# Kernel optimization log

Hardware: AMD Instinct MI355X
Metric: run time of the kernel (lower is better)

## Reference

```python
import jax, jax.numpy as jnp
import numpy as np

DIM = 1024
NH = 16        # query heads
NKV = 4        # kv heads
HD = 64        # head dim
GROUPS = NH // NKV
SPATIAL = 16
NZ = SPATIAL * SPATIAL  # 256 latent tokens with 2D structure
SOFT_CAP = 50.0
SCALE = HD ** -0.5
EPS = 1e-6


def rope_2d_cos_sin(nz, hd, spatial, dtype):
    # 2D RoPE: first half of head_dim encodes row position, second half column.
    pos = jnp.arange(nz)
    row = (pos // spatial).astype(jnp.float32)
    col = (pos % spatial).astype(jnp.float32)
    quarter = hd // 4
    inv_freq = 1.0 / (10000.0 ** (jnp.arange(quarter, dtype=jnp.float32) / quarter))
    f_row = row[:, None] * inv_freq[None, :]   # (nz, hd/4)
    f_col = col[:, None] * inv_freq[None, :]   # (nz, hd/4)
    emb = jnp.concatenate([f_row, f_col], axis=-1)      # (nz, hd/2)
    emb = jnp.concatenate([emb, emb], axis=-1)          # (nz, hd)
    return jnp.cos(emb).astype(dtype), jnp.sin(emb).astype(dtype)


def rotate_half(x):
    x1, x2 = jnp.split(x, 2, axis=-1)
    return jnp.concatenate([-x2, x1], axis=-1)


def apply_rotary(x, cos, sin):
    return x * cos + rotate_half(x) * sin


def rms_norm(x, w):
    # RMSNorm over head_dim with learned per-dim scale (QKNorm)
    return x * jax.lax.rsqrt(jnp.mean(x * x, axis=-1, keepdims=True) + EPS) * w


def setup_inputs() -> dict:
    key = jax.random.key(0)
    ks = jax.random.split(key, 7)
    B, T, S = 4, 16, 264
    x = jax.random.normal(ks[0], (B, T, S, DIM), dtype=jnp.float32)
    wq = jax.random.normal(ks[1], (NH * HD, DIM), dtype=jnp.float32) * 0.02
    wk = jax.random.normal(ks[2], (NKV * HD, DIM), dtype=jnp.float32) * 0.02
    wv = jax.random.normal(ks[3], (NKV * HD, DIM), dtype=jnp.float32) * 0.02
    wo = jax.random.normal(ks[4], (DIM, NH * HD), dtype=jnp.float32) * 0.02
    q_norm_w = jnp.ones((HD,), dtype=jnp.float32)
    k_norm_w = jnp.ones((HD,), dtype=jnp.float32)
    return {"x": x, "wq": wq, "wk": wk, "wv": wv, "wo": wo,
            "q_norm_w": q_norm_w, "k_norm_w": k_norm_w}


def reference(x, wq, wk, wv, wo, q_norm_w, k_norm_w):
    B, T, S, D = x.shape
    xf = x.reshape(B * T, S, D)
    # projections (torch Linear: y = x @ W.T)
    q = (xf @ wq.T).reshape(B * T, S, NH, HD).transpose(0, 2, 1, 3)   # (BT,NH,S,HD)
    k = (xf @ wk.T).reshape(B * T, S, NKV, HD).transpose(0, 2, 1, 3)  # (BT,NKV,S,HD)
    v = (xf @ wv.T).reshape(B * T, S, NKV, HD).transpose(0, 2, 1, 3)
    # QKNorm
    q = rms_norm(q, q_norm_w)
    k = rms_norm(k, k_norm_w)
    # partial 2D RoPE on latent tokens only
    cos, sin = rope_2d_cos_sin(NZ, HD, SPATIAL, q.dtype)
    cos = cos[None, None]  # (1,1,NZ,HD)
    sin = sin[None, None]
    q = jnp.concatenate([apply_rotary(q[:, :, :NZ], cos, sin), q[:, :, NZ:]], axis=2)
    k = jnp.concatenate([apply_rotary(k[:, :, :NZ], cos, sin), k[:, :, NZ:]], axis=2)
    # GQA: expand kv heads (repeat_interleave == jnp.repeat)
    k = jnp.repeat(k, GROUPS, axis=1)
    v = jnp.repeat(v, GROUPS, axis=1)
    # attention with soft cap
    attn = jnp.einsum("bhqd,bhkd->bhqk", q, k) * SCALE
    attn = SOFT_CAP * jnp.tanh(attn / SOFT_CAP)
    attn = jax.nn.softmax(attn, axis=-1)
    out = jnp.einsum("bhqk,bhkd->bhqd", attn, v)
    out = out.transpose(0, 2, 1, 3).reshape(B * T, S, NH * HD)
    out = out @ wo.T
    return out.reshape(B, T, S, D)
```

## Files before the change

### kernel.cpp

```cpp
#include <hip/hip_runtime.h>

typedef __bf16 bf16;
typedef __bf16 bf16x8 __attribute__((ext_vector_type(8)));
typedef float  f32x4  __attribute__((ext_vector_type(4)));
typedef float  f32x16 __attribute__((ext_vector_type(16)));
typedef unsigned int u32;

#define DIM   1024
#define NH    16
#define NKV   4
#define HD    64
#define SLEN  264
#define BTOT  64
#define MROWS (BTOT * SLEN)
#define NQKV  1536
#define NZ    256
#define VPAD  288

__device__ __forceinline__ void gl_lds16(const bf16* g, bf16* l) {
    __builtin_amdgcn_global_load_lds((__attribute__((address_space(1))) void*)(g),
                                     (__attribute__((address_space(3))) void*)(l),
                                     16, 0, 0);
}

__global__ void cvt_f32_bf16(const float* __restrict__ src, bf16* __restrict__ dst, int n) {
    int i = (blockIdx.x * 256 + threadIdx.x) * 4;
    if (i < n) {
        float4 v = *(const float4*)(src + i);
        dst[i + 0] = (bf16)v.x; dst[i + 1] = (bf16)v.y;
        dst[i + 2] = (bf16)v.z; dst[i + 3] = (bf16)v.w;
    }
}

__global__ void prep_misc(const float* __restrict__ wq, const float* __restrict__ wk,
                          const float* __restrict__ wv, const float* __restrict__ wo,
                          bf16* __restrict__ wcat, bf16* __restrict__ wobf,
                          float2* __restrict__ ctab) {
    int b = blockIdx.x, tid = threadIdx.x;
    if (b < 1536) {
        int i = (b * 256 + tid) * 4;
        const float* src; int off;
        if (i < 1024 * 1024)      { src = wq; off = i; }
        else if (i < 1280 * 1024) { src = wk; off = i - 1024 * 1024; }
        else                      { src = wv; off = i - 1280 * 1024; }
        float4 v = *(const float4*)(src + off);
        wcat[i + 0] = (bf16)v.x; wcat[i + 1] = (bf16)v.y;
        wcat[i + 2] = (bf16)v.z; wcat[i + 3] = (bf16)v.w;
    } else if (b < 2560) {
        int i = ((b - 1536) * 256 + tid) * 4;
        float4 v = *(const float4*)(wo + i);
        wobf[i + 0] = (bf16)v.x; wobf[i + 1] = (bf16)v.y;
        wobf[i + 2] = (bf16)v.z; wobf[i + 3] = (bf16)v.w;
    } else {
        int i = (b - 2560) * 256 + tid;
        int s = i >> 5, d = i & 31;
        const float LN1 = 0.5756462732485115f;
        float pos = (d < 16) ? (float)(s >> 4) : (float)(s & 15);
        float ang = pos * expf(-(float)(d & 15) * LN1);
        float sn, cs; sincosf(ang, &sn, &cs);
        ctab[i] = make_float2(cs, sn);
    }
}

__device__ __forceinline__ int xcd_swizzle(int orig, int nwg) {
    int q = nwg >> 3, r = nwg & 7;
    int xcd = orig & 7, lid = orig >> 3;
    return (xcd < r ? xcd * (q + 1) : r * (q + 1) + (xcd - r) * q) + lid;
}


#define GATE2  asm volatile("s_waitcnt vmcnt(2)" ::: "memory")
#define NOGATE do {} while (0)

#define STAGE(DST, G, H, KT) do {                                              \
    gl_lds16((G) + (size_t)((H) * 128 + rs0) * DIM + (KT) * 64 + cs0 * 8,      \
             (DST) + wid * 512);                                               \
    gl_lds16((G) + (size_t)((H) * 128 + 64 + rs0) * DIM + (KT) * 64 + cs0 * 8, \
             (DST) + 4096 + wid * 512);                                        \
} while (0)

#define PHASE(Ad, Bd, AA, KS, STAGE_STMT, GATE_STMT) do {                      \
    bf16x8 af_[4], bf_[4];                                                     \
    _Pragma("unroll")                                                          \
    for (int i_ = 0; i_ < 4; i_++) {                                           \
        af_[i_] = *(const bf16x8*)((Ad) + aRdBase + i_ * 1024 + xorv[KS]);     \
        bf_[i_] = *(const bf16x8*)((Bd) + bRdBase + i_ * 1024 + xorv[KS]);     \
    }                                                                          \
    STAGE_STMT;                                                                \
    GATE_STMT;                                                                 \
    __builtin_amdgcn_s_barrier();                                              \
    asm volatile("s_waitcnt lgkmcnt(0)" ::: "memory");                         \
    __builtin_amdgcn_sched_barrier(0);                                         \
    __builtin_amdgcn_s_setprio(1);                                             \
    _Pragma("unroll")                                                          \
    for (int i_ = 0; i_ < 4; i_++)                                             \
        _Pragma("unroll")                                                      \
        for (int n_ = 0; n_ < 4; n_++)                                         \
            acc[AA][i_][n_] = __builtin_amdgcn_mfma_f32_16x16x32_bf16(         \
                af_[i_], bf_[n_], acc[AA][i_][n_], 0, 0, 0);                   \
    __builtin_amdgcn_s_setprio(0);                                             \
    __builtin_amdgcn_s_barrier();                                              \
} while (0)

__device__ __forceinline__ void gemm256_core(const bf16* __restrict__ Ag,
                                             const bf16* __restrict__ Bg,
                                             f32x4 (&acc)[2][4][4]) {
    __shared__ __align__(16) bf16 A00[128 * 64], A01[128 * 64], A10[128 * 64], A11[128 * 64];
    __shared__ __align__(16) bf16 B00[128 * 64], B01[128 * 64], B10[128 * 64], B11[128 * 64];

    const int tid  = threadIdx.x;
    const int wid  = tid >> 6, lane = tid & 63;
    const int quad = lane >> 4, r16 = lane & 15;
    const int wm = wid & 1, wn = wid >> 1;

    const int rs0 = tid >> 3;
    const int cs0 = (tid & 7) ^ (rs0 & 7);

    const int aRdBase = (wm * 64 + r16) * 64;
    const int bRdBase = ((wn & 1) * 64 + r16) * 64;
    const int xorv[2] = { (quad ^ (r16 & 7)) * 8, ((4 + quad) ^ (r16 & 7)) * 8 };

    const bf16* Bd0 = (wn & 2) ? B01 : B00;
    const bf16* Bd1 = (wn & 2) ? B11 : B10;

    STAGE(A00, Ag, 0, 0);
    STAGE(A01, Ag, 1, 0);
    STAGE(B00, Bg, 0, 0);
    STAGE(B01, Bg, 1, 0);
    STAGE(A10, Ag, 0, 1);
    GATE2;
    __builtin_amdgcn_s_barrier();

#pragma unroll 1
    for (int it = 0; it < 8; ++it) {
        const int t1 = 2 * it + 1;
        int t2 = 2 * it + 2; if (t2 > 15) t2 = 15;
        int t3 = 2 * it + 3; if (t3 > 15) t3 = 15;
        PHASE(A00, Bd0, 0, 0, STAGE(A11, Ag, 1, t1), NOGATE);
        PHASE(A00, Bd0, 0, 1, STAGE(B10, Bg, 0, t1), NOGATE);
        PHASE(A01, Bd0, 1, 0, STAGE(B11, Bg, 1, t1), NOGATE);
        PHASE(A01, Bd0, 1, 1, STAGE(A00, Ag, 0, t2), GATE2);
        PHASE(A10, Bd1, 0, 0, STAGE(A01, Ag, 1, t2), NOGATE);
        PHASE(A10, Bd1, 0, 1, STAGE(B00, Bg, 0, t2), NOGATE);
        PHASE(A11, Bd1, 1, 0, STAGE(B01, Bg, 1, t2), NOGATE);
        PHASE(A11, Bd1, 1, 1, STAGE(A10, Ag, 0, t3), GATE2);
    }
}

__global__ __launch_bounds__(512) void gemm_qkv(const bf16* __restrict__ A,
                                                const bf16* __restrict__ Bw,
                                                bf16* __restrict__ out,
                                                const float* __restrict__ qw,
                                                const float* __restrict__ kw,
                                                const float2* __restrict__ ctab) {
    const int nwg = (MROWS / 256) * (NQKV / 256);
    int wg = xcd_swizzle(blockIdx.x, nwg);
    const int bm = wg / 6, bn = wg - bm * 6;

    f32x4 acc[2][4][4];
#pragma unroll
    for (int a = 0; a < 2; a++)
#pragma unroll
        for (int i = 0; i < 4; i++)
#pragma unroll
            for (int n = 0; n < 4; n++) acc[a][i][n] = (f32x4){0.f, 0.f, 0.f, 0.f};

    gemm256_core(A + (size_t)bm * 256 * DIM, Bw + (size_t)bn * 256 * DIM, acc);

    const int tid  = threadIdx.x;
    const int wid  = tid >> 6, lane = tid & 63;
    const int quad = lane >> 4, r16 = lane & 15;
    const int wm = wid & 1, wn = wid >> 1;
    const int colbase = bn * 256 + wn * 64;
    const int rowb    = bm * 256 + wm * 64;

    if (bn < 5) {
        const float* w = (bn < 4) ? qw : kw;
        float wreg[4];
#pragma unroll
        for (int n = 0; n < 4; n++) wreg[n] = w[n * 16 + r16];
#pragma unroll
        for (int a = 0; a < 2; a++)
#pragma unroll
            for (int i = 0; i < 4; i++)
#pragma unroll
                for (int r = 0; r < 4; r++) {
                    float ss = 0.f;
#pragma unroll
                    for (int n = 0; n < 4; n++) ss += acc[a][i][n][r] * acc[a][i][n][r];
                    ss += __shfl_xor(ss, 1, 64);
                    ss += __shfl_xor(ss, 2, 64);
                    ss += __shfl_xor(ss, 4, 64);
                    ss += __shfl_xor(ss, 8, 64);
                    float rms = rsqrtf(ss * (1.f / 64.f) + 1e-6f);
                    float xv[4];
#pragma unroll
                    for (int n = 0; n < 4; n++) xv[n] = acc[a][i][n][r] * rms * wreg[n];
                    int gm = rowb + a * 128 + i * 16 + quad * 4 + r;
                    int s = gm % SLEN;
                    if (s < NZ) {
                        float2 cs0 = ctab[s * 32 + r16];
                        float2 cs1 = ctab[s * 32 + 16 + r16];
                        float a0 = xv[0] * cs0.x - xv[2] * cs0.y;
                        float a2 = xv[2] * cs0.x + xv[0] * cs0.y;
                        float a1 = xv[1] * cs1.x - xv[3] * cs1.y;
                        float a3 = xv[3] * cs1.x + xv[1] * cs1.y;
                        xv[0] = a0; xv[1] = a1; xv[2] = a2; xv[3] = a3;
                    }
                    size_t rowoff = (size_t)gm * NQKV + colbase + r16;
#pragma unroll
                    for (int n = 0; n < 4; n++) out[rowoff + n * 16] = (bf16)xv[n];
                }
    } else {
#pragma unroll
        for (int a = 0; a < 2; a++)
#pragma unroll
            for (int i = 0; i < 4; i++)
#pragma unroll
                for (int r = 0; r < 4; r++) {
                    int gm = rowb + a * 128 + i * 16 + quad * 4 + r;
                    size_t rowoff = (size_t)gm * NQKV + colbase + r16;
#pragma unroll
                    for (int n = 0; n < 4; n++) out[rowoff + n * 16] = (bf16)acc[a][i][n][r];
                }
    }
}

#define GEMM_STAGE_PTRS(Mptr, tileRow, K, P)                                   \
    const bf16* P[4];                                                          \
    {                                                                          \
        _Pragma("unroll")                                                      \
        for (int k = 0; k < 4; k++) {                                          \
            int s = k * 256 + tid;                                             \
            int r = s >> 3, cp = s & 7;                                        \
            int c = cp ^ (r & 7);                                              \
            P[k] = (Mptr) + (size_t)((tileRow) + r) * (K) + c * 8;             \
        }                                                                      \
    }

__device__ __forceinline__ int swz(int row, int chunk) {
    return row * 64 + ((chunk ^ (row & 7)) * 8);
}

__global__ __launch_bounds__(256) void gemm_bt(const bf16* __restrict__ A,
                                               const bf16* __restrict__ Bw,
                                               float* __restrict__ Cout) {
    __shared__ __align__(16) bf16 As[128 * 64];
    __shared__ __align__(16) bf16 Bs[128 * 64];
    const int tid  = threadIdx.x;
    const int wid  = tid >> 6, lane = tid & 63;
    const int quad = lane >> 4, r16 = lane & 15;
    const int bid = blockIdx.x;
    const int g = bid / 32, rr = bid - g * 32;
    const int bm = g * 4 + (rr & 3), bn = rr >> 2;
    const int wm = wid & 1, wn = wid >> 1;

    GEMM_STAGE_PTRS(A,  bm * 128, DIM, Ap)
    GEMM_STAGE_PTRS(Bw, bn * 128, DIM, Bp)

    f32x4 acc[4][4];
#pragma unroll
    for (int i = 0; i < 4; i++)
#pragma unroll
        for (int j = 0; j < 4; j++) acc[i][j] = (f32x4){0.f, 0.f, 0.f, 0.f};

    for (int k0 = 0; k0 < DIM; k0 += 64) {
        __syncthreads();
#pragma unroll
        for (int k = 0; k < 4; k++) {
            gl_lds16(Ap[k] + k0, As + (k * 256 + wid * 64) * 8);
            gl_lds16(Bp[k] + k0, Bs + (k * 256 + wid * 64) * 8);
        }
        __syncthreads();
#pragma unroll
        for (int ks = 0; ks < 2; ks++) {
            bf16x8 a[4], b[4];
#pragma unroll
            for (int i = 0; i < 4; i++) {
                a[i] = *(const bf16x8*)&As[swz(wm * 64 + i * 16 + r16, ks * 4 + quad)];
                b[i] = *(const bf16x8*)&Bs[swz(wn * 64 + i * 16 + r16, ks * 4 + quad)];
            }
#pragma unroll
            for (int i = 0; i < 4; i++)
#pragma unroll
                for (int j = 0; j < 4; j++)
                    acc[i][j] = __builtin_amdgcn_mfma_f32_16x16x32_bf16(a[i], b[j], acc[i][j], 0, 0, 0);
        }
    }

#pragma unroll
    for (int i = 0; i < 4; i++)
#pragma unroll
        for (int j = 0; j < 4; j++)
#pragma unroll
            for (int r = 0; r < 4; r++) {
                int gm = bm * 128 + wm * 64 + i * 16 + quad * 4 + r;
                int gn = bn * 128 + wn * 64 + j * 16 + r16;
                Cout[(size_t)gm * DIM + gn] = acc[i][j][r];
            }
}

__global__ __launch_bounds__(256) void vtrans_kernel(const bf16* __restrict__ qkv,
                                                     bf16* __restrict__ vt) {
    __shared__ bf16 Ls[64 * 272];
    const int tid = threadIdx.x;
    const int b = blockIdx.x, bt = b >> 2, kv = b & 3;
    const int part = tid >> 5;
    const int rr   = tid & 31;
#pragma unroll
    for (int pass = 0; pass < 9; ++pass) {
        int row = pass * 32 + rr;
        if (row < SLEN) {
            bf16x8 v = *(const bf16x8*)(qkv + (size_t)(bt * SLEN + row) * NQKV + 1280 + kv * 64 + part * 8);
#pragma unroll
            for (int j = 0; j < 8; j++) Ls[(part * 8 + j) * 272 + row] = v[j];
        }
    }
    __syncthreads();
    const int d = tid >> 2, seg = tid & 3;
    size_t obase = ((size_t)b * 64 + d) * VPAD;
#pragma unroll
    for (int m = 0; m < 9; ++m) {
        int col = seg * 72 + m * 8;
        bf16x8 o;
#pragma unroll
        for (int j = 0; j < 8; j++) {
            int s = col + j;
            o[j] = (s < SLEN) ? Ls[d * 272 + s] : (bf16)0.f;
        }
        *(bf16x8*)(vt + obase + col) = o;
    }
}

__global__ __launch_bounds__(256) void attn_kernel(const bf16* __restrict__ qkv,
                                                   const bf16* __restrict__ vt,
                                                   bf16* __restrict__ aout) {
    __shared__ float invL[4][32];
    const int tid = threadIdx.x;
    const int wid = tid >> 6, lane = tid & 63;
    const int l31 = lane & 31, hi = lane >> 5;
    const int qp = blockIdx.x;
    const int kv = blockIdx.y, bt = blockIdx.z;
    const int h = kv * 4 + wid;

    int q0 = qp * 32 + l31;
    int qcl = q0 < SLEN ? q0 : SLEN - 1;
    const bf16* qbase = qkv + (size_t)(bt * SLEN + qcl) * NQKV + h * HD + hi * 8;
    bf16x8 qb[4];
#pragma unroll
    for (int s = 0; s < 4; s++) qb[s] = *(const bf16x8*)(qbase + s * 16);

    const bf16* kbase = qkv + (size_t)bt * SLEN * NQKV + 1024 + kv * HD + hi * 8;
    const bf16* vbase = vt + (size_t)(bt * 4 + kv) * HD * VPAD;

    bf16x8 nka[4];
    {
        const bf16* kp = kbase + (size_t)l31 * NQKV;
#pragma unroll
        for (int s = 0; s < 4; s++) nka[s] = *(const bf16x8*)(kp + s * 16);
    }

    f32x16 oacc[2];
#pragma unroll
    for (int r = 0; r < 16; r++) { oacc[0][r] = 0.f; oacc[1][r] = 0.f; }
    float lsum = 0.f;

    for (int c = 0; c < 9; ++c) {
        bf16x8 ka[4];
#pragma unroll
        for (int s = 0; s < 4; s++) ka[s] = nka[s];
        if (c < 8) {
            int key = (c + 1) * 32 + l31;
            int kc = key < SLEN ? key : SLEN - 1;
            const bf16* kp = kbase + (size_t)kc * NQKV;
#pragma unroll
            for (int s = 0; s < 4; s++) nka[s] = *(const bf16x8*)(kp + s * 16);
        }
        bf16x8 vb[2][2];
#pragma unroll
        for (int dt = 0; dt < 2; dt++)
#pragma unroll
            for (int st = 0; st < 2; st++)
                vb[dt][st] = *(const bf16x8*)(vbase + (size_t)(dt * 32 + l31) * VPAD + c * 32 + st * 16 + hi * 8);

        f32x16 sacc;
#pragma unroll
        for (int r = 0; r < 16; r++) sacc[r] = 0.f;
#pragma unroll
        for (int s = 0; s < 4; s++)
            sacc = __builtin_amdgcn_mfma_f32_32x32x16_bf16(ka[s], qb[s], sacc, 0, 0, 0);

        float p[16];
#pragma unroll
        for (int r = 0; r < 16; ++r) {
            int key = c * 32 + (r & 3) + 8 * (r >> 2) + 4 * hi;
            float sc = sacc[r];
            float z = sc * 0.0025f;
            float z2 = z * z;
            float poly = fmaf(z2, fmaf(z2, 0.133333333f, -0.333333333f), 1.f);
            float pv = exp2f(sc * 0.18033688f * poly);
            pv = (key < SLEN) ? pv : 0.f;
            p[r] = pv;
            lsum += pv;
        }
#pragma unroll
        for (int st = 0; st < 2; st++) {
            u32 wA, wB, wC, wD;
            asm("v_cvt_pk_bf16_f32 %0, %1, %2" : "=v"(wA) : "v"(p[st*8+0]), "v"(p[st*8+1]));
            asm("v_cvt_pk_bf16_f32 %0, %1, %2" : "=v"(wB) : "v"(p[st*8+2]), "v"(p[st*8+3]));
            asm("v_cvt_pk_bf16_f32 %0, %1, %2" : "=v"(wC) : "v"(p[st*8+4]), "v"(p[st*8+5]));
            asm("v_cvt_pk_bf16_f32 %0, %1, %2" : "=v"(wD) : "v"(p[st*8+6]), "v"(p[st*8+7]));
            asm volatile("v_permlane32_swap_b32 %0, %1" : "+v"(wA), "+v"(wC));
            asm volatile("v_permlane32_swap_b32 %0, %1" : "+v"(wB), "+v"(wD));
            union { u32 u[4]; bf16x8 v; } pa;
            pa.u[0] = wA; pa.u[1] = wB; pa.u[2] = wC; pa.u[3] = wD;
#pragma unroll
            for (int dt = 0; dt < 2; dt++)
                oacc[dt] = __builtin_amdgcn_mfma_f32_32x32x16_bf16(pa.v, vb[dt][st], oacc[dt], 0, 0, 0);
        }
    }

    lsum += __shfl_xor(lsum, 32, 64);
    invL[wid][l31] = 1.f / lsum;
#pragma unroll
    for (int r = 0; r < 16; ++r) {
        int qloc = (r & 3) + 8 * (r >> 2) + 4 * hi;
        int q = qp * 32 + qloc;
        if (q < SLEN) {
            float inv = invL[wid][qloc];
            size_t base = (size_t)(bt * SLEN + q) * (NH * HD) + h * HD + l31;
            aout[base]      = (bf16)(oacc[0][r] * inv);
            aout[base + 32] = (bf16)(oacc[1][r] * inv);
        }
    }
}

extern "C" void kernel_launch(void* const* d_in, const int* in_sizes, int n_in,
                              void* d_out, int out_size, void* d_ws, size_t ws_size,
                              hipStream_t stream) {
    const float* x   = (const float*)d_in[0];
    const float* wq  = (const float*)d_in[1];
    const float* wk  = (const float*)d_in[2];
    const float* wv  = (const float*)d_in[3];
    const float* wo  = (const float*)d_in[4];
    const float* qnw = (const float*)d_in[5];
    const float* knw = (const float*)d_in[6];

    bf16* xbf  = (bf16*)d_ws;
    bf16* wcat = xbf  + (size_t)MROWS * DIM;
    bf16* wobf = wcat + (size_t)NQKV * DIM;
    bf16* qkv  = wobf + (size_t)DIM * DIM;
    bf16* vt   = qkv  + (size_t)MROWS * NQKV;
    float2* ctab = (float2*)(vt + (size_t)BTOT * NKV * HD * VPAD);
    bf16* aout = xbf;

    prep_misc<<<2592, 256, 0, stream>>>(wq, wk, wv, wo, wcat, wobf, ctab);
    cvt_f32_bf16<<<(MROWS * DIM) / 1024, 256, 0, stream>>>(x, xbf, MROWS * DIM);

    gemm_qkv<<<(MROWS / 256) * (NQKV / 256), 512, 0, stream>>>(xbf, wcat, qkv, qnw, knw, ctab);
    vtrans_kernel<<<BTOT * NKV, 256, 0, stream>>>(qkv, vt);
    attn_kernel<<<dim3(9, NKV, BTOT), 256, 0, stream>>>(qkv, vt, aout);
    gemm_bt<<<(MROWS / 128) * (DIM / 128), 256, 0, stream>>>(aout, wobf, (float*)d_out);
}
```

Baseline: 338.6 us.

## Stage K/V tiles through double-buffered LDS shared by all heads in attention

The attention kernel now loads 64-key K and V tiles into double-buffered, XOR-swizzled shared memory with async global-to-LDS loads. The four query-head waves of a block share each tile instead of each wave loading K and V from global memory on its own. The tanh soft-cap polynomial is also refactored into a single polynomial in sc^2 to save a multiply. This adds block-wide barriers and LDS traffic in exchange for less redundant global traffic.

Result: no change. 335.3 us (-1.0%).

```diff
diff --git a/kernel.cpp b/kernel.cpp
--- a/kernel.cpp
+++ b/kernel.cpp
@@ -68,7 +68,6 @@
     return (xcd < r ? xcd * (q + 1) : r * (q + 1) + (xcd - r) * q) + lid;
 }
 
-
 #define GATE2  asm volatile("s_waitcnt vmcnt(2)" ::: "memory")
 #define NOGATE do {} while (0)
 
@@ -335,7 +334,10 @@
 __global__ __launch_bounds__(256) void attn_kernel(const bf16* __restrict__ qkv,
                                                    const bf16* __restrict__ vt,
                                                    bf16* __restrict__ aout) {
+    __shared__ __align__(16) bf16 Kb[2][64 * 64];
+    __shared__ __align__(16) bf16 Vb[2][64 * 64];
     __shared__ float invL[4][32];
+
     const int tid = threadIdx.x;
     const int wid = tid >> 6, lane = tid & 63;
     const int l31 = lane & 31, hi = lane >> 5;
@@ -350,75 +352,86 @@
 #pragma unroll
     for (int s = 0; s < 4; s++) qb[s] = *(const bf16x8*)(qbase + s * 16);
 
-    const bf16* kbase = qkv + (size_t)bt * SLEN * NQKV + 1024 + kv * HD + hi * 8;
-    const bf16* vbase = vt + (size_t)(bt * 4 + kv) * HD * VPAD;
-
-    bf16x8 nka[4];
-    {
-        const bf16* kp = kbase + (size_t)l31 * NQKV;
-#pragma unroll
-        for (int s = 0; s < 4; s++) nka[s] = *(const bf16x8*)(kp + s * 16);
-    }
+    const int r0  = tid >> 3;
+    const int r1  = r0 + 32;
+    const int kc0 = (tid & 7) ^ (r0 & 7);
+    const bf16* kg = qkv + (size_t)bt * SLEN * NQKV + 1024 + kv * 64 + kc0 * 8;
+    const bf16* vg = vt + (size_t)(bt * 4 + kv) * HD * VPAD;
+
+#define STAGEP(PB, P64) do {                                                     \
+    int kr0 = (P64) + r0; if (kr0 > SLEN - 1) kr0 = SLEN - 1;                    \
+    int kr1 = (P64) + r1; if (kr1 > SLEN - 1) kr1 = SLEN - 1;                    \
+    gl_lds16(kg + (size_t)kr0 * NQKV, &Kb[PB][tid * 8]);                         \
+    gl_lds16(kg + (size_t)kr1 * NQKV, &Kb[PB][(tid + 256) * 8]);                 \
+    int vo = (P64) + kc0 * 8; if (vo > VPAD - 8) vo = VPAD - 8;                  \
+    gl_lds16(vg + (size_t)r0 * VPAD + vo, &Vb[PB][tid * 8]);                     \
+    gl_lds16(vg + (size_t)r1 * VPAD + vo, &Vb[PB][(tid + 256) * 8]);             \
+} while (0)
+
+    const int xorb = l31 & 7;
+    int koff[4];
+#pragma unroll
+    for (int s = 0; s < 4; s++) koff[s] = l31 * 64 + (((s * 2 + hi) ^ xorb) * 8);
 
     f32x16 oacc[2];
 #pragma unroll
     for (int r = 0; r < 16; r++) { oacc[0][r] = 0.f; oacc[1][r] = 0.f; }
     float lsum = 0.f;
 
-    for (int c = 0; c < 9; ++c) {
-        bf16x8 ka[4];
-#pragma unroll
-        for (int s = 0; s < 4; s++) ka[s] = nka[s];
-        if (c < 8) {
-            int key = (c + 1) * 32 + l31;
-            int kc = key < SLEN ? key : SLEN - 1;
-            const bf16* kp = kbase + (size_t)kc * NQKV;
-#pragma unroll
-            for (int s = 0; s < 4; s++) nka[s] = *(const bf16x8*)(kp + s * 16);
-        }
-        bf16x8 vb[2][2];
-#pragma unroll
-        for (int dt = 0; dt < 2; dt++)
-#pragma unroll
-            for (int st = 0; st < 2; st++)
-                vb[dt][st] = *(const bf16x8*)(vbase + (size_t)(dt * 32 + l31) * VPAD + c * 32 + st * 16 + hi * 8);
-
-        f32x16 sacc;
-#pragma unroll
-        for (int r = 0; r < 16; r++) sacc[r] = 0.f;
-#pragma unroll
-        for (int s = 0; s < 4; s++)
-            sacc = __builtin_amdgcn_mfma_f32_32x32x16_bf16(ka[s], qb[s], sacc, 0, 0, 0);
-
-        float p[16];
-#pragma unroll
-        for (int r = 0; r < 16; ++r) {
-            int key = c * 32 + (r & 3) + 8 * (r >> 2) + 4 * hi;
-            float sc = sacc[r];
-            float z = sc * 0.0025f;
-            float z2 = z * z;
-            float poly = fmaf(z2, fmaf(z2, 0.133333333f, -0.333333333f), 1.f);
-            float pv = exp2f(sc * 0.18033688f * poly);
-            pv = (key < SLEN) ? pv : 0.f;
-            p[r] = pv;
-            lsum += pv;
-        }
-#pragma unroll
-        for (int st = 0; st < 2; st++) {
-            u32 wA, wB, wC, wD;
-            asm("v_cvt_pk_bf16_f32 %0, %1, %2" : "=v"(wA) : "v"(p[st*8+0]), "v"(p[st*8+1]));
-            asm("v_cvt_pk_bf16_f32 %0, %1, %2" : "=v"(wB) : "v"(p[st*8+2]), "v"(p[st*8+3]));
-            asm("v_cvt_pk_bf16_f32 %0, %1, %2" : "=v"(wC) : "v"(p[st*8+4]), "v"(p[st*8+5]));
-            asm("v_cvt_pk_bf16_f32 %0, %1, %2" : "=v"(wD) : "v"(p[st*8+6]), "v"(p[st*8+7]));
-            asm volatile("v_permlane32_swap_b32 %0, %1" : "+v"(wA), "+v"(wC));
-            asm volatile("v_permlane32_swap_b32 %0, %1" : "+v"(wB), "+v"(wD));
-            union { u32 u[4]; bf16x8 v; } pa;
-            pa.u[0] = wA; pa.u[1] = wB; pa.u[2] = wC; pa.u[3] = wD;
-#pragma unroll
-            for (int dt = 0; dt < 2; dt++)
-                oacc[dt] = __builtin_amdgcn_mfma_f32_32x32x16_bf16(pa.v, vb[dt][st], oacc[dt], 0, 0, 0);
-        }
-    }
+    STAGEP(0, 0);
+    __syncthreads();
+
+#pragma unroll 1
+    for (int p = 0; p < 5; ++p) {
+        const int pb = p & 1;
+        if (p < 4) STAGEP(pb ^ 1, (p + 1) * 64);
+        const int hmax = (p == 4) ? 1 : 2;
+        for (int hh = 0; hh < hmax; ++hh) {
+            const bf16* Kp = &Kb[pb][hh * 2048];
+            f32x16 sacc;
+#pragma unroll
+            for (int r = 0; r < 16; r++) sacc[r] = 0.f;
+#pragma unroll
+            for (int s = 0; s < 4; s++) {
+                bf16x8 ka = *(const bf16x8*)(Kp + koff[s]);
+                sacc = __builtin_amdgcn_mfma_f32_32x32x16_bf16(ka, qb[s], sacc, 0, 0, 0);
+            }
+            const int keyb = p * 64 + hh * 32;
+            float pr[16];
+#pragma unroll
+            for (int r = 0; r < 16; ++r) {
+                float sc = sacc[r];
+                float t = sc * sc;
+                float w = fmaf(t, 9.392546e-13f, -3.7570183e-7f);
+                w = fmaf(t, w, 0.18033688f);
+                float pv = exp2f(sc * w);
+                int key = keyb + (r & 3) + 8 * (r >> 2) + 4 * hi;
+                pv = (key < SLEN) ? pv : 0.f;
+                pr[r] = pv;
+                lsum += pv;
+            }
+#pragma unroll
+            for (int st = 0; st < 2; st++) {
+                u32 wA, wB, wC, wD;
+                asm("v_cvt_pk_bf16_f32 %0, %1, %2" : "=v"(wA) : "v"(pr[st*8+0]), "v"(pr[st*8+1]));
+                asm("v_cvt_pk_bf16_f32 %0, %1, %2" : "=v"(wB) : "v"(pr[st*8+2]), "v"(pr[st*8+3]));
+                asm("v_cvt_pk_bf16_f32 %0, %1, %2" : "=v"(wC) : "v"(pr[st*8+4]), "v"(pr[st*8+5]));
+                asm("v_cvt_pk_bf16_f32 %0, %1, %2" : "=v"(wD) : "v"(pr[st*8+6]), "v"(pr[st*8+7]));
+                asm volatile("v_permlane32_swap_b32 %0, %1" : "+v"(wA), "+v"(wC));
+                asm volatile("v_permlane32_swap_b32 %0, %1" : "+v"(wB), "+v"(wD));
+                union { u32 u[4]; bf16x8 v; } pa;
+                pa.u[0] = wA; pa.u[1] = wB; pa.u[2] = wC; pa.u[3] = wD;
+#pragma unroll
+                for (int dt = 0; dt < 2; dt++) {
+                    bf16x8 vbf = *(const bf16x8*)(&Vb[pb][(dt * 32 + l31) * 64 +
+                                         (((hh * 4 + st * 2 + hi) ^ xorb) * 8)]);
+                    oacc[dt] = __builtin_amdgcn_mfma_f32_32x32x16_bf16(pa.v, vbf, oacc[dt], 0, 0, 0);
+                }
+            }
+        }
+        if (p < 4) __syncthreads();
+    }
+#undef STAGEP
 
     lsum += __shfl_xor(lsum, 32, 64);
     invL[wid][l31] = 1.f / lsum;
```
